# Performance work log

Hardware: AMD Instinct MI355X
Metric: run time of the kernel (lower is better)

The kernel has to match this reference:

```python
import jax, jax.numpy as jnp
import numpy as np
import math

B, N = 1, 768
C_S, C_Z, C_H, H, P_QK, P_V = 256, 128, 128, 8, 8, 12
EPS, INF, LN_EPS = 1e-8, 1e5, 1e-5


def _quat_to_rot(q):
    # q: [..., 4] normalized quaternion (w, x, y, z) -> [..., 3, 3]
    w, x, y, z = jnp.moveaxis(q, -1, 0)
    r = jnp.stack([
        1 - 2 * (y * y + z * z), 2 * (x * y - w * z), 2 * (x * z + w * y),
        2 * (x * y + w * z), 1 - 2 * (x * x + z * z), 2 * (y * z - w * x),
        2 * (x * z - w * y), 2 * (y * z + w * x), 1 - 2 * (x * x + y * y),
    ], axis=-1)
    return r.reshape(q.shape[:-1] + (3, 3))


def _ln(x, g, b):
    mu = x.mean(-1, keepdims=True)
    var = ((x - mu) ** 2).mean(-1, keepdims=True)
    return (x - mu) * jax.lax.rsqrt(var + LN_EPS) * g + b


def setup_inputs():
    key = jax.random.key(0)
    ks = jax.random.split(key, 20)
    inp = {}
    inp['s'] = jax.random.normal(ks[0], (B, N, C_S), jnp.float32)
    inp['p'] = jax.random.normal(ks[1], (B, N, N, C_Z), jnp.float32)
    q = jax.random.normal(ks[2], (B, N, 4), jnp.float32)
    inp['rot'] = _quat_to_rot(q / jnp.linalg.norm(q, axis=-1, keepdims=True))
    inp['trans'] = 10.0 * jax.random.normal(ks[3], (B, N, 3), jnp.float32)
    inp['mask'] = jnp.ones((B, N), jnp.float32)
    concat_dim = H * C_H + H * P_V * 4 + H * C_Z
    dims = {'q': (H * C_H, C_S), 'kv': (2 * H * C_H, C_S), 'qp': (H * P_QK * 3, C_S),
            'kvp': (H * (P_QK + P_V) * 3, C_S), 'pb': (H, C_Z), 'o': (C_S, concat_dim),
            't1': (C_S, C_S), 't2': (C_S, C_S), 't3': (C_S, C_S), 'bb': (6, C_S)}
    i = 4
    for nm, (do, di) in dims.items():
        k1, k2 = jax.random.split(ks[i]); i += 1
        inp['W' + nm] = 0.02 * jax.random.normal(k1, (do, di), jnp.float32)
        inp['b' + nm] = 0.02 * jax.random.normal(k2, (do,), jnp.float32)
    inp['head_w'] = 0.1 * jax.random.normal(ks[i], (H,), jnp.float32)
    inp['g1'] = jnp.ones((C_S,), jnp.float32)
    inp['be1'] = jnp.zeros((C_S,), jnp.float32)
    inp['g2'] = jnp.ones((C_S,), jnp.float32)
    inp['be2'] = jnp.zeros((C_S,), jnp.float32)
    return inp


def reference(s, p, rot, trans, mask, Wq, bq, Wkv, bkv, Wqp, bqp, Wkvp, bkvp,
              Wpb, bpb, Wo, bo, Wt1, bt1, Wt2, bt2, Wt3, bt3, Wbb, bbb,
              head_w, g1, be1, g2, be2):
    # ---------------- Invariant Point Attention ----------------
    q = (s @ Wq.T + bq).reshape(B, N, H, C_H)
    kv = (s @ Wkv.T + bkv).reshape(B, N, H, 2 * C_H)
    k, v = kv[..., :C_H], kv[..., C_H:]
    # points: linear output is coordinate-major (x-block, y-block, z-block)
    qp = (s @ Wqp.T + bqp).reshape(B, N, 3, H, P_QK)
    qp = jnp.einsum('bnij,bnjhp->bnhpi', rot, qp) + trans[:, :, None, None, :]
    kvp = (s @ Wkvp.T + bkvp).reshape(B, N, 3, H, P_QK + P_V)
    kvp = jnp.einsum('bnij,bnjhp->bnhpi', rot, kvp) + trans[:, :, None, None, :]
    kp, vp = kvp[..., :P_QK, :], kvp[..., P_QK:, :]
    bias_p = p @ Wpb.T + bpb  # [B,N,N,H]
    a = jnp.einsum('bihc,bjhc->bhij', q, k) * math.sqrt(1.0 / (3 * C_H))
    a = a + math.sqrt(1.0 / 3) * jnp.transpose(bias_p, (0, 3, 1, 2))
    d2 = ((qp[:, :, None] - kp[:, None]) ** 2).sum(-1)  # [B,N,N,H,Pqk]
    hw = jax.nn.softplus(head_w) * math.sqrt(1.0 / (3 * (P_QK * 9.0 / 2)))
    pt_att = -0.5 * (d2 * hw[None, None, None, :, None]).sum(-1)  # [B,N,N,H]
    m2 = mask[:, :, None] * mask[:, None, :]
    a = a + jnp.transpose(pt_att, (0, 3, 1, 2)) + (INF * (m2 - 1.0))[:, None]
    att = jax.nn.softmax(a, axis=-1)  # [B,H,N,N]
    o = jnp.einsum('bhij,bjhc->bihc', att, v).reshape(B, N, H * C_H)
    opt = jnp.einsum('bhij,bjhpx->bihpx', att, vp)  # [B,N,H,Pv,3] global
    opt = jnp.einsum('bnji,bnhpj->bnhpi', rot, opt - trans[:, :, None, None, :])
    opt_norm = jnp.sqrt((opt ** 2).sum(-1) + EPS).reshape(B, N, H * P_V)
    opt_flat = jnp.moveaxis(opt.reshape(B, N, H * P_V, 3), -1, -2).reshape(B, N, 3 * H * P_V)
    opair = jnp.einsum('bhij,bijz->bihz', att, p).reshape(B, N, H * C_Z)
    ipa_out = jnp.concatenate([o, opt_flat, opt_norm, opair], -1) @ Wo.T + bo
    # residual + dropout(eval: identity) + LayerNorm
    s1 = _ln(s + ipa_out, g1, be1)
    # ---------------- StructureTransition (1 layer) ----------------
    x = jax.nn.relu(s1 @ Wt1.T + bt1)
    x = jax.nn.relu(x @ Wt2.T + bt2)
    s2 = _ln(s1 + (x @ Wt3.T + bt3), g2, be2)
    # ---------------- BackboneUpdate + masked quaternion compose ----------------
    upd = (s2 @ Wbb.T + bbb) * mask[..., None]  # [B,N,6]
    qvec = jnp.concatenate([jnp.ones(upd.shape[:-1] + (1,), upd.dtype), upd[..., :3]], -1)
    qvec = qvec / jnp.linalg.norm(qvec, axis=-1, keepdims=True)
    rot_new = jnp.einsum('bnij,bnjk->bnik', rot, _quat_to_rot(qvec))
    trans_new = trans + jnp.einsum('bnij,bnj->bni', rot, upd[..., 3:])
    return (s2, rot_new, trans_new)
```

## Files before the change

### kernel.cpp

```cpp
#include <hip/hip_runtime.h>
#include <hip/hip_bf16.h>
#include <math.h>

#define NN 768
#define CS 256
#define CZ 128
#define CH 128
#define HH 8
#define PQK 8
#define PV 12
#define CONCAT 2432
#define ATT_HSTRIDE (768*768)

typedef __bf16 v8bf __attribute__((ext_vector_type(8)));
typedef float  v4f  __attribute__((ext_vector_type(4)));

__device__ inline unsigned short f2bf(float f) {
    union { float f; unsigned u; } v; v.f = f;
    unsigned r = v.u + 0x7FFFu + ((v.u >> 16) & 1u);
    return (unsigned short)(r >> 16);
}
__device__ inline float bf2f(unsigned short u) {
    union { unsigned u; float f; } v; v.u = ((unsigned)u) << 16; return v.f;
}

#define NCVT 9
struct CvtDesc {
    const float* src[NCVT];
    unsigned short* dst[NCVT];
    int nelem[NCVT];
    int blk_start[NCVT + 1];
};

__global__ __launch_bounds__(256) void cvt_many(CvtDesc d)
{
    int b = blockIdx.x;
    int seg = 0;
    #pragma unroll
    for (int i = 0; i < NCVT - 1; i++) if (b >= d.blk_start[i + 1]) seg = i + 1;
    int local = b - d.blk_start[seg];
    int base = local * 2048 + threadIdx.x;
    const float* s = d.src[seg];
    unsigned short* o = d.dst[seg];
    int n = d.nelem[seg];
    #pragma unroll
    for (int r = 0; r < 8; r++) {
        int idx = base + r * 256;
        if (idx < n) o[idx] = f2bf(s[idx]);
    }
}

template<int SPLITK, int MODE, int RELU>
__global__ __launch_bounds__(256) void mfma_gemm(
    const unsigned short* __restrict__ A,
    const unsigned short* __restrict__ W,
    const float* __restrict__ bias,
    float* __restrict__ C,
    unsigned short* __restrict__ Cb,
    int D, int K, int ldc)
{
    __shared__ unsigned short As[64][40];
    __shared__ unsigned short Ws[64][40];
    int tid = threadIdx.x;
    int bi = blockIdx.y * 64;
    int bd = blockIdx.x * 64;
    int kpb = K / SPLITK;
    int k0b = blockIdx.z * kpb;
    int lane = tid & 63;
    int wid = tid >> 6;
    int wr = (wid >> 1) * 32, wc = (wid & 1) * 32;
    v4f acc[2][2] = {};
    int lrow = tid >> 2;
    int lcol = (tid & 3) * 8;
    const unsigned short* Ap = A + (size_t)(bi + lrow) * K + lcol;
    const unsigned short* Wp = W + (size_t)(bd + lrow) * K + lcol;
    bool wv = (bd + lrow) < D;
    int fr = lane & 15, fc = (lane >> 4) * 8;

    for (int k0 = k0b; k0 < k0b + kpb; k0 += 32) {
        *(int4*)&As[lrow][lcol] = *(const int4*)(Ap + k0);
        int4 wz = {0, 0, 0, 0};
        *(int4*)&Ws[lrow][lcol] = wv ? *(const int4*)(Wp + k0) : wz;
        __syncthreads();
        v8bf a0 = *(const v8bf*)&As[wr + fr][fc];
        v8bf a1 = *(const v8bf*)&As[wr + 16 + fr][fc];
        v8bf b0 = *(const v8bf*)&Ws[wc + fr][fc];
        v8bf b1 = *(const v8bf*)&Ws[wc + 16 + fr][fc];
        acc[0][0] = __builtin_amdgcn_mfma_f32_16x16x32_bf16(a0, b0, acc[0][0], 0, 0, 0);
        acc[0][1] = __builtin_amdgcn_mfma_f32_16x16x32_bf16(a0, b1, acc[0][1], 0, 0, 0);
        acc[1][0] = __builtin_amdgcn_mfma_f32_16x16x32_bf16(a1, b0, acc[1][0], 0, 0, 0);
        acc[1][1] = __builtin_amdgcn_mfma_f32_16x16x32_bf16(a1, b1, acc[1][1], 0, 0, 0);
        __syncthreads();
    }
    int mrow = (lane >> 4) * 4;
    #pragma unroll
    for (int mi = 0; mi < 2; mi++) {
        #pragma unroll
        for (int ni = 0; ni < 2; ni++) {
            int d = bd + wc + ni * 16 + fr;
            if (d < D) {
                #pragma unroll
                for (int r = 0; r < 4; r++) {
                    int m = bi + wr + mi * 16 + mrow + r;
                    float v = acc[mi][ni][r];
                    if (SPLITK > 1) {
                        atomicAdd(&C[(size_t)m * ldc + d], v);
                    } else {
                        v += bias[d];
                        if (RELU) v = fmaxf(v, 0.f);
                        if (MODE != 2) C[(size_t)m * ldc + d] = v;
                        if (MODE >= 1) Cb[(size_t)m * ldc + d] = f2bf(v);
                    }
                }
            }
        }
    }
}

__global__ __launch_bounds__(256) void ipa_init_kernel(
    const float* __restrict__ bo, float* __restrict__ ipa)
{
    ipa[blockIdx.x * 256 + threadIdx.x] = bo[threadIdx.x];
}

__global__ void prep_kernel(const float* __restrict__ head_w, float* __restrict__ hw8)
{
    int t = threadIdx.x;
    if (t < HH) {
        float x = head_w[t];
        float sp = (x > 20.f) ? x : log1pf(expf(x));
        hw8[t] = sp * 0.09622504486493764f;
    }
}

__global__ void rotate_kernel(
    const float* __restrict__ qpraw, const float* __restrict__ kvpraw,
    const float* __restrict__ rot, const float* __restrict__ trans,
    float* __restrict__ qpb, float* __restrict__ kpb,
    unsigned short* __restrict__ qph, unsigned short* __restrict__ qpl,
    unsigned short* __restrict__ kph, unsigned short* __restrict__ kpl,
    unsigned short* __restrict__ Vc)
{
    int id = blockIdx.x*256 + threadIdx.x;
    if (id >= NN*HH*28) return;
    int i = id / (HH*28);
    int rem = id % (HH*28);
    int h = rem / 28;
    int idx = rem % 28;
    const float* R = rot + i*9;
    const float* T = trans + i*3;
    float s0, s1, s2;
    if (idx < 8) {
        s0 = qpraw[i*192 +   0 + h*8 + idx];
        s1 = qpraw[i*192 +  64 + h*8 + idx];
        s2 = qpraw[i*192 + 128 + h*8 + idx];
    } else {
        int pp = idx - 8;
        s0 = kvpraw[i*480 +   0 + h*20 + pp];
        s1 = kvpraw[i*480 + 160 + h*20 + pp];
        s2 = kvpraw[i*480 + 320 + h*20 + pp];
    }
    float ov[3];
    ov[0] = R[0]*s0 + R[1]*s1 + R[2]*s2 + T[0];
    ov[1] = R[3]*s0 + R[4]*s1 + R[5]*s2 + T[1];
    ov[2] = R[6]*s0 + R[7]*s1 + R[8]*s2 + T[2];
    if (idx < 8) {
        #pragma unroll
        for (int x = 0; x < 3; x++) {
            qpb[i*192 + h*24 + idx*3 + x] = ov[x];
            unsigned short hi = f2bf(ov[x]);
            qph[i*256 + h*32 + idx*3 + x] = hi;
            qpl[i*256 + h*32 + idx*3 + x] = f2bf(ov[x] - bf2f(hi));
        }
        if (idx == 0) {
            #pragma unroll
            for (int m = 24; m < 32; m++) { qph[i*256+h*32+m] = 0; qpl[i*256+h*32+m] = 0; }
        }
    } else if (idx < 16) {
        int pp = idx - 8;
        #pragma unroll
        for (int x = 0; x < 3; x++) {
            kpb[i*192 + h*24 + pp*3 + x] = ov[x];
            unsigned short hi = f2bf(ov[x]);
            kph[i*256 + h*32 + pp*3 + x] = hi;
            kpl[i*256 + h*32 + pp*3 + x] = f2bf(ov[x] - bf2f(hi));
        }
        if (idx == 8) {
            #pragma unroll
            for (int m = 24; m < 32; m++) { kph[i*256+h*32+m] = 0; kpl[i*256+h*32+m] = 0; }
        }
    } else {
        int ppv = idx - 16;
        #pragma unroll
        for (int x = 0; x < 3; x++)
            Vc[((size_t)h*192 + 128 + ppv*3 + x)*768 + i] = f2bf(ov[x]);
    }
}

__global__ void sq_kernel(const float* __restrict__ qpb, const float* __restrict__ kpb,
                          float* __restrict__ Qsq, float* __restrict__ Ksq)
{
    int id = blockIdx.x*256 + threadIdx.x;
    if (id >= NN*HH) return;
    const float* qq = qpb + id*24;
    const float* kk = kpb + id*24;
    float a = 0.f, b = 0.f;
    #pragma unroll
    for (int m = 0; m < 24; m++) { a += qq[m]*qq[m]; b += kk[m]*kk[m]; }
    Qsq[id] = a; Ksq[id] = b;
}

__global__ __launch_bounds__(256) void vtrans_kernel(
    const unsigned short* __restrict__ kv_bf, unsigned short* __restrict__ Vc)
{
    __shared__ unsigned short tile[32][136];
    int h = blockIdx.x & 7, jt = blockIdx.x >> 3;
    int t = threadIdx.x;
    int r = t >> 3, c0 = (t & 7) * 16;
    const unsigned short* src = kv_bf + (size_t)(jt*32 + r)*2048 + h*256 + 128 + c0;
    *(int4*)&tile[r][c0]     = *(const int4*)src;
    *(int4*)&tile[r][c0 + 8] = *(const int4*)(src + 8);
    __syncthreads();
    int c = t >> 1, jh = (t & 1) * 16;
    unsigned short tmp[16];
    #pragma unroll
    for (int k = 0; k < 16; k++) tmp[k] = tile[jh + k][c];
    unsigned short* dst = Vc + ((size_t)h*192 + c)*768 + jt*32 + jh;
    *(int4*)dst       = *(int4*)&tmp[0];
    *(int4*)(dst + 8) = *(int4*)&tmp[8];
}

__global__ __launch_bounds__(256) void logits_mfma(
    const unsigned short* __restrict__ q_bf, const unsigned short* __restrict__ kv_bf,
    const unsigned short* __restrict__ qph, const unsigned short* __restrict__ qpl,
    const unsigned short* __restrict__ kph, const unsigned short* __restrict__ kpl,
    const float* __restrict__ Qsq, const float* __restrict__ Ksq,
    const float* __restrict__ mask, const float* __restrict__ hw8,
    float* __restrict__ att)
{
    __shared__ unsigned short Qs[64][136];
    __shared__ unsigned short Ks[64][136];
    __shared__ unsigned short Aph[64][40], Apl[64][40], Bph[64][40], Bpl[64][40];
    __shared__ float Qss[64], Kss[64], Mi[64], Mj[64];
    int h = blockIdx.z;
    int i0 = blockIdx.y * 64, j0 = blockIdx.x * 64;
    int tid = threadIdx.x, lane = tid & 63, wid = tid >> 6;
    int wr = (wid >> 1) * 32, wc = (wid & 1) * 32;
    int r = tid >> 2, cq = (tid & 3) * 32;
    const unsigned short* qg = q_bf  + (size_t)(i0 + r)*1024 + h*128 + cq;
    const unsigned short* kg = kv_bf + (size_t)(j0 + r)*2048 + h*256 + cq;
    #pragma unroll
    for (int kk = 0; kk < 4; kk++) {
        *(int4*)&Qs[r][cq + kk*8] = *(const int4*)(qg + kk*8);
        *(int4*)&Ks[r][cq + kk*8] = *(const int4*)(kg + kk*8);
    }
    int cp = (tid & 3) * 8;
    *(int4*)&Aph[r][cp] = *(const int4*)(qph + (size_t)(i0 + r)*256 + h*32 + cp);
    *(int4*)&Apl[r][cp] = *(const int4*)(qpl + (size_t)(i0 + r)*256 + h*32 + cp);
    *(int4*)&Bph[r][cp] = *(const int4*)(kph + (size_t)(j0 + r)*256 + h*32 + cp);
    *(int4*)&Bpl[r][cp] = *(const int4*)(kpl + (size_t)(j0 + r)*256 + h*32 + cp);
    if (tid < 64) {
        Qss[tid] = Qsq[(i0 + tid)*8 + h];
        Kss[tid] = Ksq[(j0 + tid)*8 + h];
        Mi[tid] = mask[i0 + tid];
        Mj[tid] = mask[j0 + tid];
    }
    __syncthreads();
    int fr = lane & 15, fc = (lane >> 4) * 8;
    v4f aqk[2][2] = {}, ap[2][2] = {};
    #pragma unroll
    for (int ks = 0; ks < 4; ks++) {
        v8bf a0 = *(const v8bf*)&Qs[wr + fr][ks*32 + fc];
        v8bf a1 = *(const v8bf*)&Qs[wr + 16 + fr][ks*32 + fc];
        v8bf b0 = *(const v8bf*)&Ks[wc + fr][ks*32 + fc];
        v8bf b1 = *(const v8bf*)&Ks[wc + 16 + fr][ks*32 + fc];
        aqk[0][0] = __builtin_amdgcn_mfma_f32_16x16x32_bf16(a0, b0, aqk[0][0], 0, 0, 0);
        aqk[0][1] = __builtin_amdgcn_mfma_f32_16x16x32_bf16(a0, b1, aqk[0][1], 0, 0, 0);
        aqk[1][0] = __builtin_amdgcn_mfma_f32_16x16x32_bf16(a1, b0, aqk[1][0], 0, 0, 0);
        aqk[1][1] = __builtin_amdgcn_mfma_f32_16x16x32_bf16(a1, b1, aqk[1][1], 0, 0, 0);
    }
    {
        v8bf ah0 = *(const v8bf*)&Aph[wr + fr][fc];
        v8bf ah1 = *(const v8bf*)&Aph[wr + 16 + fr][fc];
        v8bf al0 = *(const v8bf*)&Apl[wr + fr][fc];
        v8bf al1 = *(const v8bf*)&Apl[wr + 16 + fr][fc];
        v8bf bh0 = *(const v8bf*)&Bph[wc + fr][fc];
        v8bf bh1 = *(const v8bf*)&Bph[wc + 16 + fr][fc];
        v8bf bl0 = *(const v8bf*)&Bpl[wc + fr][fc];
        v8bf bl1 = *(const v8bf*)&Bpl[wc + 16 + fr][fc];
        ap[0][0] = __builtin_amdgcn_mfma_f32_16x16x32_bf16(ah0, bh0, ap[0][0], 0, 0, 0);
        ap[0][1] = __builtin_amdgcn_mfma_f32_16x16x32_bf16(ah0, bh1, ap[0][1], 0, 0, 0);
        ap[1][0] = __builtin_amdgcn_mfma_f32_16x16x32_bf16(ah1, bh0, ap[1][0], 0, 0, 0);
        ap[1][1] = __builtin_amdgcn_mfma_f32_16x16x32_bf16(ah1, bh1, ap[1][1], 0, 0, 0);
        ap[0][0] = __builtin_amdgcn_mfma_f32_16x16x32_bf16(ah0, bl0, ap[0][0], 0, 0, 0);
        ap[0][1] = __builtin_amdgcn_mfma_f32_16x16x32_bf16(ah0, bl1, ap[0][1], 0, 0, 0);
        ap[1][0] = __builtin_amdgcn_mfma_f32_16x16x32_bf16(ah1, bl0, ap[1][0], 0, 0, 0);
        ap[1][1] = __builtin_amdgcn_mfma_f32_16x16x32_bf16(ah1, bl1, ap[1][1], 0, 0, 0);
        ap[0][0] = __builtin_amdgcn_mfma_f32_16x16x32_bf16(al0, bh0, ap[0][0], 0, 0, 0);
        ap[0][1] = __builtin_amdgcn_mfma_f32_16x16x32_bf16(al0, bh1, ap[0][1], 0, 0, 0);
        ap[1][0] = __builtin_amdgcn_mfma_f32_16x16x32_bf16(al1, bh0, ap[1][0], 0, 0, 0);
        ap[1][1] = __builtin_amdgcn_mfma_f32_16x16x32_bf16(al1, bh1, ap[1][1], 0, 0, 0);
    }
    float hw = hw8[h];
    const float scale_qk = 0.05103103630798288f;
    int mrow = (lane >> 4) * 4;
    #pragma unroll
    for (int mi = 0; mi < 2; mi++) {
        #pragma unroll
        for (int ni = 0; ni < 2; ni++) {
            int jl = wc + ni*16 + fr;
            #pragma unroll
            for (int rr = 0; rr < 4; rr++) {
                int il = wr + mi*16 + mrow + rr;
                size_t aidx = (size_t)h*ATT_HSTRIDE + (size_t)(i0 + il)*768 + (j0 + jl);
                att[aidx] = aqk[mi][ni][rr]*scale_qk + hw*ap[mi][ni][rr]
                          - 0.5f*hw*(Qss[il] + Kss[jl])
                          + 100000.0f*(Mi[il]*Mj[jl] - 1.0f);
            }
        }
    }
}

__global__ __launch_bounds__(256) void fused_p2_kernel(
    const float* __restrict__ att0,
    const float* __restrict__ p,
    const float* __restrict__ Wpb, const float* __restrict__ bpb,
    unsigned short* __restrict__ att_bf,
    float* __restrict__ linv,
    unsigned short* __restrict__ concat)
{
    __shared__ unsigned short ptile[64][136];
    __shared__ unsigned short pT[128][88];
    __shared__ unsigned short wt[16][72];
    __shared__ unsigned short Wpb16[16][136];
    __shared__ float bpb_s[8], m8[8], inv_s[8], lsum_w[4][8];

    int i = blockIdx.x;
    int tid = threadIdx.x, lane = tid & 63, wid = tid >> 6;
    int fr = lane & 15, fc = (lane >> 4) * 8;
    int mrow = (lane >> 4) * 4;

    for (int idx = tid; idx < 16*72; idx += 256) wt[idx / 72][idx % 72] = 0;
    for (int idx = tid; idx < 16*136; idx += 256) {
        int h = idx / 136, z = idx % 136;
        Wpb16[h][z] = (h < 8 && z < 128) ? f2bf(Wpb[h*128 + z]) : 0;
    }
    if (tid < 8) bpb_s[tid] = bpb[tid];

    {
        const float* abase = att0 + (size_t)i*768;
        #pragma unroll
        for (int hh = 0; hh < 2; hh++) {
            int h = wid*2 + hh;
            const float* row = abase + (size_t)h*ATT_HSTRIDE;
            float m = -3.0e38f;
            #pragma unroll
            for (int e = 0; e < 12; e++) m = fmaxf(m, row[lane + e*64]);
            #pragma unroll
            for (int d2 = 1; d2 < 64; d2 <<= 1) m = fmaxf(m, __shfl_xor(m, d2));
            if (lane == 0) m8[h] = m;
        }
    }

    const float* pbase = p + (size_t)i*98304;
    float4 pfA[4], pfB[4];
    #pragma unroll
    for (int r = 0; r < 4; r++) {
        int idx = r*256 + tid;
        const float* src = pbase + (idx >> 4)*128 + (idx & 15)*8;
        pfA[r] = *(const float4*)src;
        pfB[r] = *(const float4*)(src + 4);
    }

    v4f accop[2] = {};
    float lacc[4] = {0.f, 0.f, 0.f, 0.f};
    const float sqrt13 = 0.57735026918962576f;

    for (int t64 = 0; t64 < 12; t64++) {
        int j0 = t64 * 64;
        #pragma unroll
        for (int r = 0; r < 4; r++) {
            int idx = r*256 + tid;
            int j = idx >> 4, zo = (idx & 15) * 8;
            unsigned u0 = (unsigned)f2bf(pfA[r].x) | ((unsigned)f2bf(pfA[r].y) << 16);
            unsigned u1 = (unsigned)f2bf(pfA[r].z) | ((unsigned)f2bf(pfA[r].w) << 16);
            unsigned u2 = (unsigned)f2bf(pfB[r].x) | ((unsigned)f2bf(pfB[r].y) << 16);
            unsigned u3 = (unsigned)f2bf(pfB[r].z) | ((unsigned)f2bf(pfB[r].w) << 16);
            int4 val; val.x = (int)u0; val.y = (int)u1; val.z = (int)u2; val.w = (int)u3;
            *(int4*)&ptile[j][zo] = val;
        }
        if (t64 < 11) {
            int j0n = j0 + 64;
            #pragma unroll
            for (int r = 0; r < 4; r++) {
                int idx = r*256 + tid;
                const float* src = pbase + (size_t)(j0n + (idx >> 4))*128 + (idx & 15)*8;
                pfA[r] = *(const float4*)src;
                pfB[r] = *(const float4*)(src + 4);
            }
        }
        __syncthreads();

        float a0v[4];
        if (mrow < 8) {
            int j = 16*wid + fr;
            #pragma unroll
            for (int r = 0; r < 4; r++)
                a0v[r] = att0[((size_t)(mrow + r)*768 + i)*768 + j0 + j];
        }

        #pragma unroll
        for (int rep = 0; rep < 2; rep++) {
            int item = rep*256 + tid;
            int zp = item & 63, jg = item >> 6;
            unsigned v[8];
            #pragma unroll
            for (int k = 0; k < 8; k++)
                v[k] = *(const unsigned*)&ptile[jg*8 + k][zp*2];
            unsigned r0[4], r1[4];
            #pragma unroll
            for (int q = 0; q < 4; q++) {
                unsigned a = v[2*q], b = v[2*q + 1];
                r0[q] = (a & 0xffffu) | ((b & 0xffffu) << 16);
                r1[q] = (a >> 16) | (b & 0xffff0000u);
            }
            int4 w0; w0.x = (int)r0[0]; w0.y = (int)r0[1]; w0.z = (int)r0[2]; w0.w = (int)r0[3];
            int4 w1; w1.x = (int)r1[0]; w1.y = (int)r1[1]; w1.z = (int)r1[2]; w1.w = (int)r1[3];
            *(int4*)&pT[2*zp][jg*8]     = w0;
            *(int4*)&pT[2*zp + 1][jg*8] = w1;
        }

        v4f bd = {};
        #pragma unroll
        for (int ks = 0; ks < 4; ks++) {
            v8bf a = *(const v8bf*)&Wpb16[fr][ks*32 + fc];
            v8bf b = *(const v8bf*)&ptile[16*wid + fr][ks*32 + fc];
            bd = __builtin_amdgcn_mfma_f32_16x16x32_bf16(a, b, bd, 0, 0, 0);
        }

        if (mrow < 8) {
            int j = 16*wid + fr;
            float w8[4];
            #pragma unroll
            for (int r = 0; r < 4; r++) {
                int h = mrow + r;
                float L = a0v[r] + sqrt13*(bd[r] + bpb_s[h]);
                w8[r] = expf(fminf(L - m8[h], 60.f));
            }
            #pragma unroll
            for (int r = 0; r < 4; r++) {
                int h = mrow + r;
                unsigned short wb = f2bf(w8[r]);
                wt[h][j] = wb;
                att_bf[((size_t)h*768 + i)*768 + j0 + j] = wb;
            }
            #pragma unroll
            for (int m = 1; m < 16; m <<= 1) {
                #pragma unroll
                for (int r = 0; r < 4; r++) w8[r] += __shfl_xor(w8[r], m);
            }
            #pragma unroll
            for (int r = 0; r < 4; r++) lacc[r] += w8[r];
        }
        __syncthreads();

        #pragma unroll
        for (int mm = 0; mm < 2; mm++) {
            #pragma unroll
            for (int ks = 0; ks < 2; ks++) {
                v8bf a = *(const v8bf*)&pT[(2*wid + mm)*16 + fr][ks*32 + fc];
                v8bf b = *(const v8bf*)&wt[fr][ks*32 + fc];
                accop[mm] = __builtin_amdgcn_mfma_f32_16x16x32_bf16(a, b, accop[mm], 0, 0, 0);
            }
        }
    }

    __syncthreads();
    if (fr == 0 && mrow < 8) {
        #pragma unroll
        for (int r = 0; r < 4; r++) lsum_w[wid][mrow + r] = lacc[r];
    }
    __syncthreads();
    if (tid < 8) {
        float l = lsum_w[0][tid] + lsum_w[1][tid] + lsum_w[2][tid] + lsum_w[3][tid];
        float iv = 1.0f / l;
        inv_s[tid] = iv;
        linv[(size_t)tid*768 + i] = iv;
    }
    __syncthreads();
    if (fr < 8) {
        int h = fr;
        float iv = inv_s[h];
        #pragma unroll
        for (int mm = 0; mm < 2; mm++) {
            #pragma unroll
            for (int r = 0; r < 4; r++) {
                int z = (2*wid + mm)*16 + mrow + r;
                concat[(size_t)i*CONCAT + 1408 + h*128 + z] = f2bf(accop[mm][r] * iv);
            }
        }
    }
}

__global__ __launch_bounds__(256) void attvc_mfma(
    const unsigned short* __restrict__ att_bf, const unsigned short* __restrict__ Vc,
    const float* __restrict__ linv,
    unsigned short* __restrict__ concat, float* __restrict__ optb)
{
    __shared__ unsigned short As[64][72];
    __shared__ unsigned short Bs[64][72];
    int h = blockIdx.z;
    int i0 = blockIdx.y * 64, nd0 = blockIdx.x * 64;
    int tid = threadIdx.x, lane = tid & 63, wid = tid >> 6;
    int wr = (wid >> 1) * 32, wc = (wid & 1) * 32;
    int r = tid >> 2, c8 = (tid & 3) * 16;
    int fr = lane & 15, fc = (lane >> 4) * 8;
    v4f acc[2][2] = {};
    for (int k0 = 0; k0 < 768; k0 += 64) {
        const unsigned short* ag = att_bf + ((size_t)h*768 + i0 + r)*768 + k0 + c8;
        const unsigned short* bg = Vc + ((size_t)h*192 + nd0 + r)*768 + k0 + c8;
        *(int4*)&As[r][c8]     = *(const int4*)ag;
        *(int4*)&As[r][c8 + 8] = *(const int4*)(ag + 8);
        *(int4*)&Bs[r][c8]     = *(const int4*)bg;
        *(int4*)&Bs[r][c8 + 8] = *(const int4*)(bg + 8);
        __syncthreads();
        #pragma unroll
        for (int ks = 0; ks < 2; ks++) {
            v8bf a0 = *(const v8bf*)&As[wr + fr][ks*32 + fc];
            v8bf a1 = *(const v8bf*)&As[wr + 16 + fr][ks*32 + fc];
            v8bf b0 = *(const v8bf*)&Bs[wc + fr][ks*32 + fc];
            v8bf b1 = *(const v8bf*)&Bs[wc + 16 + fr][ks*32 + fc];
            acc[0][0] = __builtin_amdgcn_mfma_f32_16x16x32_bf16(a0, b0, acc[0][0], 0, 0, 0);
            acc[0][1] = __builtin_amdgcn_mfma_f32_16x16x32_bf16(a0, b1, acc[0][1], 0, 0, 0);
            acc[1][0] = __builtin_amdgcn_mfma_f32_16x16x32_bf16(a1, b0, acc[1][0], 0, 0, 0);
            acc[1][1] = __builtin_amdgcn_mfma_f32_16x16x32_bf16(a1, b1, acc[1][1], 0, 0, 0);
        }
        __syncthreads();
    }
    int mrow = (lane >> 4) * 4;
    float lv[2][4];
    #pragma unroll
    for (int mi = 0; mi < 2; mi++) {
        int ibase = i0 + wr + mi*16 + mrow;
        float4 l4 = *(const float4*)&linv[(size_t)h*768 + ibase];
        lv[mi][0] = l4.x; lv[mi][1] = l4.y; lv[mi][2] = l4.z; lv[mi][3] = l4.w;
    }
    #pragma unroll
    for (int mi = 0; mi < 2; mi++) {
        #pragma unroll
        for (int ni = 0; ni < 2; ni++) {
            int d = nd0 + wc + ni*16 + fr;
            #pragma unroll
            for (int rr = 0; rr < 4; rr++) {
                int i = i0 + wr + mi*16 + mrow + rr;
                float v = acc[mi][ni][rr] * lv[mi][rr];
                if (d < 128) {
                    concat[(size_t)i*CONCAT + h*128 + d] = f2bf(v);
                } else if (d < 164) {
                    optb[(size_t)i*288 + h*36 + (d - 128)] = v;
                }
            }
        }
    }
}

__global__ void optfinal_kernel(
    const float* __restrict__ optb, const float* __restrict__ rot,
    const float* __restrict__ trans, unsigned short* __restrict__ concat)
{
    int id = blockIdx.x*256 + threadIdx.x;
    if (id >= NN*96) return;
    int i = id / 96;
    int hp = id % 96;
    const float* ob = optb + i*288 + hp*3;
    float y0 = ob[0] - trans[i*3+0];
    float y1 = ob[1] - trans[i*3+1];
    float y2 = ob[2] - trans[i*3+2];
    const float* R = rot + i*9;
    float o0 = R[0]*y0 + R[3]*y1 + R[6]*y2;
    float o1 = R[1]*y0 + R[4]*y1 + R[7]*y2;
    float o2 = R[2]*y0 + R[5]*y1 + R[8]*y2;
    float nrm = sqrtf(o0*o0 + o1*o1 + o2*o2 + 1e-8f);
    unsigned short* cb = concat + (size_t)i*CONCAT;
    cb[1024 +   0 + hp] = f2bf(o0);
    cb[1024 +  96 + hp] = f2bf(o1);
    cb[1024 + 192 + hp] = f2bf(o2);
    cb[1312 + hp] = f2bf(nrm);
}

template<int BF>
__global__ __launch_bounds__(256) void add_ln_kernel(
    const float* __restrict__ A, const float* __restrict__ Bv,
    const float* __restrict__ g, const float* __restrict__ be,
    float* __restrict__ out, unsigned short* __restrict__ outb)
{
    int i = blockIdx.x, t = threadIdx.x;
    float x = A[i*256 + t] + Bv[i*256 + t];
    __shared__ float red[4];
    float v = x;
    #pragma unroll
    for (int m = 1; m < 64; m <<= 1) v += __shfl_xor(v, m);
    if ((t & 63) == 0) red[t >> 6] = v;
    __syncthreads();
    float mu = (red[0] + red[1] + red[2] + red[3]) * (1.0f/256.0f);
    __syncthreads();
    float d = x - mu;
    float v2 = d*d;
    #pragma unroll
    for (int m = 1; m < 64; m <<= 1) v2 += __shfl_xor(v2, m);
    if ((t & 63) == 0) red[t >> 6] = v2;
    __syncthreads();
    float var = (red[0] + red[1] + red[2] + red[3]) * (1.0f/256.0f);
    float o = d * (1.0f/sqrtf(var + 1e-5f)) * g[t] + be[t];
    out[i*256 + t] = o;
    if (BF) outb[i*256 + t] = f2bf(o);
}

__global__ __launch_bounds__(256) void upd_kernel(
    const float* __restrict__ s2, const float* __restrict__ Wbb,
    const float* __restrict__ bbb, const float* __restrict__ mask,
    float* __restrict__ upd)
{
    int i = blockIdx.x, t = threadIdx.x;
    __shared__ float row[256];
    row[t] = s2[i*256 + t];
    __syncthreads();
    if (t < 6) {
        float acc = bbb[t];
        #pragma unroll 8
        for (int c = 0; c < 256; c++) acc += row[c]*Wbb[t*256 + c];
        upd[i*6 + t] = acc * mask[i];
    }
}

__global__ void frame_kernel(
    const float* __restrict__ upd, const float* __restrict__ rot,
    const float* __restrict__ trans, float* __restrict__ rot_out,
    float* __restrict__ trans_out)
{
    int i = blockIdx.x*64 + threadIdx.x;
    if (i >= NN) return;
    float u0 = upd[i*6+0], u1 = upd[i*6+1], u2 = upd[i*6+2];
    float t0 = upd[i*6+3], t1 = upd[i*6+4], t2 = upd[i*6+5];
    float n = sqrtf(1.f + u0*u0 + u1*u1 + u2*u2);
    float w = 1.f/n, x = u0/n, y = u1/n, z = u2/n;
    float R[3][3];
    R[0][0] = 1.f - 2.f*(y*y + z*z); R[0][1] = 2.f*(x*y - w*z);       R[0][2] = 2.f*(x*z + w*y);
    R[1][0] = 2.f*(x*y + w*z);       R[1][1] = 1.f - 2.f*(x*x + z*z); R[1][2] = 2.f*(y*z - w*x);
    R[2][0] = 2.f*(x*z - w*y);       R[2][1] = 2.f*(y*z + w*x);       R[2][2] = 1.f - 2.f*(x*x + y*y);
    const float* Ri = rot + i*9;
    #pragma unroll
    for (int a = 0; a < 3; a++) {
        #pragma unroll
        for (int b = 0; b < 3; b++) {
            float acc = 0.f;
            #pragma unroll
            for (int j = 0; j < 3; j++) acc += Ri[a*3+j]*R[j][b];
            rot_out[i*9 + a*3 + b] = acc;
        }
        trans_out[i*3 + a] = trans[i*3 + a] + Ri[a*3+0]*t0 + Ri[a*3+1]*t1 + Ri[a*3+2]*t2;
    }
}

extern "C" void kernel_launch(void* const* d_in, const int* in_sizes, int n_in,
                              void* d_out, int out_size, void* d_ws, size_t ws_size,
                              hipStream_t stream)
{
    const float* s      = (const float*)d_in[0];
    const float* p      = (const float*)d_in[1];
    const float* rot    = (const float*)d_in[2];
    const float* trans  = (const float*)d_in[3];
    const float* mask   = (const float*)d_in[4];
    const float* Wq     = (const float*)d_in[5];
    const float* bq     = (const float*)d_in[6];
    const float* Wkv    = (const float*)d_in[7];
    const float* bkv    = (const float*)d_in[8];
    const float* Wqp    = (const float*)d_in[9];
    const float* bqp    = (const float*)d_in[10];
    const float* Wkvp   = (const float*)d_in[11];
    const float* bkvp   = (const float*)d_in[12];
    const float* Wpb    = (const float*)d_in[13];
    const float* bpb    = (const float*)d_in[14];
    const float* Wo     = (const float*)d_in[15];
    const float* bo     = (const float*)d_in[16];
    const float* Wt1    = (const float*)d_in[17];
    const float* bt1    = (const float*)d_in[18];
    const float* Wt2    = (const float*)d_in[19];
    const float* bt2    = (const float*)d_in[20];
    const float* Wt3    = (const float*)d_in[21];
    const float* bt3    = (const float*)d_in[22];
    const float* Wbb    = (const float*)d_in[23];
    const float* bbb    = (const float*)d_in[24];
    const float* head_w = (const float*)d_in[25];
    const float* g1     = (const float*)d_in[26];
    const float* be1    = (const float*)d_in[27];
    const float* g2     = (const float*)d_in[28];
    const float* be2    = (const float*)d_in[29];

    float* out = (float*)d_out;
    char*  wsb = (char*)d_ws;

    size_t off = 0;
    auto alloc = [&](size_t bytes) -> char* {
        char* ptr = wsb + off;
        off += (bytes + 255) & ~(size_t)255;
        return ptr;
    };
    float* qpraw   = (float*)alloc((size_t)NN*192*4);
    float* kvpraw  = (float*)alloc((size_t)NN*480*4);
    float* qpb     = (float*)alloc((size_t)NN*192*4);
    float* kpb     = (float*)alloc((size_t)NN*192*4);
    float* Qsq     = (float*)alloc((size_t)NN*8*4);
    float* Ksq     = (float*)alloc((size_t)NN*8*4);
    float* hw8     = (float*)alloc(64);
    float* att     = (float*)alloc((size_t)8*768*768*4);
    float* optb    = (float*)alloc((size_t)NN*288*4);
    float* ipa     = (float*)alloc((size_t)NN*256*4);
    float* s1      = (float*)alloc((size_t)NN*256*4);
    float* y3      = (float*)alloc((size_t)NN*256*4);
    float* updb    = (float*)alloc((size_t)NN*6*4);
    float* linv    = (float*)alloc((size_t)8*768*4);
    unsigned short* s_bf    = (unsigned short*)alloc((size_t)NN*256*2);
    unsigned short* Wq_bf   = (unsigned short*)alloc((size_t)1024*256*2);
    unsigned short* Wkv_bf  = (unsigned short*)alloc((size_t)2048*256*2);
    unsigned short* Wqp_bf  = (unsigned short*)alloc((size_t)192*256*2);
    unsigned short* Wkvp_bf = (unsigned short*)alloc((size_t)480*256*2);
    unsigned short* Wo_bf   = (unsigned short*)alloc((size_t)256*2432*2);
    unsigned short* Wt1_bf  = (unsigned short*)alloc((size_t)256*256*2);
    unsigned short* Wt2_bf  = (unsigned short*)alloc((size_t)256*256*2);
    unsigned short* Wt3_bf  = (unsigned short*)alloc((size_t)256*256*2);
    unsigned short* q_bf    = (unsigned short*)alloc((size_t)NN*1024*2);
    unsigned short* kv_bf   = (unsigned short*)alloc((size_t)NN*2048*2);
    unsigned short* qph     = (unsigned short*)alloc((size_t)NN*256*2);
    unsigned short* qpl     = (unsigned short*)alloc((size_t)NN*256*2);
    unsigned short* kph     = (unsigned short*)alloc((size_t)NN*256*2);
    unsigned short* kpl     = (unsigned short*)alloc((size_t)NN*256*2);
    unsigned short* Vc      = (unsigned short*)alloc((size_t)8*192*768*2);
    unsigned short* att_bf  = (unsigned short*)alloc((size_t)8*768*768*2);
    unsigned short* concat  = (unsigned short*)alloc((size_t)NN*CONCAT*2);
    unsigned short* s1b     = (unsigned short*)alloc((size_t)NN*256*2);
    unsigned short* x1b     = (unsigned short*)alloc((size_t)NN*256*2);
    unsigned short* x2b     = (unsigned short*)alloc((size_t)NN*256*2);

    CvtDesc cd;
    const float* csrc[NCVT]    = {s, Wq, Wkv, Wqp, Wkvp, Wo, Wt1, Wt2, Wt3};
    unsigned short* cdst[NCVT] = {s_bf, Wq_bf, Wkv_bf, Wqp_bf, Wkvp_bf, Wo_bf, Wt1_bf, Wt2_bf, Wt3_bf};
    int csz[NCVT] = {NN*256, 1024*256, 2048*256, 192*256, 480*256, 256*2432, 256*256, 256*256, 256*256};
    int cum = 0;
    for (int i2 = 0; i2 < NCVT; i2++) {
        cd.src[i2] = csrc[i2]; cd.dst[i2] = cdst[i2]; cd.nelem[i2] = csz[i2];
        cd.blk_start[i2] = cum;
        cum += (csz[i2] + 2047) / 2048;
    }
    cd.blk_start[NCVT] = cum;
    cvt_many<<<cum, 256, 0, stream>>>(cd);

    mfma_gemm<1,2,0><<<dim3(16,12), 256, 0, stream>>>(s_bf, Wq_bf,   bq,   nullptr, q_bf,  1024, 256, 1024);
    mfma_gemm<1,2,0><<<dim3(32,12), 256, 0, stream>>>(s_bf, Wkv_bf,  bkv,  nullptr, kv_bf, 2048, 256, 2048);
    mfma_gemm<1,0,0><<<dim3(3,12),  256, 0, stream>>>(s_bf, Wqp_bf,  bqp,  qpraw,  nullptr, 192, 256, 192);
    mfma_gemm<1,0,0><<<dim3(8,12),  256, 0, stream>>>(s_bf, Wkvp_bf, bkvp, kvpraw, nullptr, 480, 256, 480);

    prep_kernel<<<1, 64, 0, stream>>>(head_w, hw8);
    rotate_kernel<<<(NN*HH*28 + 255)/256, 256, 0, stream>>>(
        qpraw, kvpraw, rot, trans, qpb, kpb, qph, qpl, kph, kpl, Vc);
    sq_kernel<<<(NN*HH + 255)/256, 256, 0, stream>>>(qpb, kpb, Qsq, Ksq);
    vtrans_kernel<<<8*24, 256, 0, stream>>>(kv_bf, Vc);

    logits_mfma<<<dim3(12, 12, 8), 256, 0, stream>>>(
        q_bf, kv_bf, qph, qpl, kph, kpl, Qsq, Ksq, mask, hw8, att);
    fused_p2_kernel<<<768, 256, 0, stream>>>(att, p, Wpb, bpb, att_bf, linv, concat);

    attvc_mfma<<<dim3(3, 12, 8), 256, 0, stream>>>(att_bf, Vc, linv, concat, optb);
    optfinal_kernel<<<(NN*96 + 255)/256, 256, 0, stream>>>(optb, rot, trans, concat);

    ipa_init_kernel<<<768, 256, 0, stream>>>(bo, ipa);
    mfma_gemm<4,0,0><<<dim3(4,12,4), 256, 0, stream>>>(concat, Wo_bf, nullptr, ipa, nullptr, 256, 2432, 256);
    add_ln_kernel<1><<<768, 256, 0, stream>>>(s, ipa, g1, be1, s1, s1b);

    mfma_gemm<1,2,1><<<dim3(4,12), 256, 0, stream>>>(s1b, Wt1_bf, bt1, nullptr, x1b, 256, 256, 256);
    mfma_gemm<1,2,1><<<dim3(4,12), 256, 0, stream>>>(x1b, Wt2_bf, bt2, nullptr, x2b, 256, 256, 256);
    mfma_gemm<1,0,0><<<dim3(4,12), 256, 0, stream>>>(x2b, Wt3_bf, bt3, y3, nullptr, 256, 256, 256);
    add_ln_kernel<0><<<768, 256, 0, stream>>>(s1, y3, g2, be2, out, nullptr);

    upd_kernel<<<768, 256, 0, stream>>>(out, Wbb, bbb, mask, updb);
    frame_kernel<<<12, 64, 0, stream>>>(updb, rot, trans, out + (size_t)NN*256, out + (size_t)NN*256 + (size_t)NN*9);
}
```

Baseline: 213.7 us.

## Fuse projections, squared-norm, softplus, opt-final and frame kernels; drop pT transpose

Merges the four input projection GEMMs into one grouped launch and folds the squared-norm, head-weight softplus, output-point rotation and frame update into neighbouring kernels. This removes several small launches and their intermediate buffers. The pair-bias kernel no longer builds a transposed copy in shared memory; it reads columns directly for the MFMA B operand and keeps Wpb in registers. It also switches to the fast exp and native bf16 conversions. Squared norms are now rebuilt from the hi/lo bf16 split, which may slightly change precision, and the strided shared-memory column reads may cause bank conflicts.

```diff
diff --git a/kernel.cpp b/kernel.cpp
--- a/kernel.cpp
+++ b/kernel.cpp
@@ -13,6 +13,7 @@
 #define ATT_HSTRIDE (768*768)
 
 typedef __bf16 v8bf __attribute__((ext_vector_type(8)));
+typedef __bf16 v4bf __attribute__((ext_vector_type(4)));
 typedef float  v4f  __attribute__((ext_vector_type(4)));
 
 __device__ inline unsigned short f2bf(float f) {
@@ -47,6 +48,77 @@
     for (int r = 0; r < 8; r++) {
         int idx = base + r * 256;
         if (idx < n) o[idx] = f2bf(s[idx]);
+    }
+}
+
+struct ProjDesc {
+    const unsigned short* W[4];
+    const float* bias[4];
+    unsigned short* dstb[4];
+    float* dstf[4];
+    int D[4];
+    int ldc[4];
+    int mode[4];
+    int blk_start[5];
+};
+
+__global__ __launch_bounds__(256) void proj_all(const unsigned short* __restrict__ A, ProjDesc d)
+{
+    __shared__ unsigned short As[64][40];
+    __shared__ unsigned short Ws[64][40];
+    int bx = blockIdx.x;
+    int seg = 0;
+    #pragma unroll
+    for (int q = 0; q < 3; q++) if (bx >= d.blk_start[q + 1]) seg = q + 1;
+    int bd = (bx - d.blk_start[seg]) * 64;
+    int bi = blockIdx.y * 64;
+    const unsigned short* W = d.W[seg];
+    int D = d.D[seg], ldc = d.ldc[seg];
+
+    int tid = threadIdx.x, lane = tid & 63, wid = tid >> 6;
+    int wr = (wid >> 1) * 32, wc = (wid & 1) * 32;
+    v4f acc[2][2] = {};
+    int lrow = tid >> 2, lcol = (tid & 3) * 8;
+    const unsigned short* Ap = A + (size_t)(bi + lrow) * 256 + lcol;
+    const unsigned short* Wp = W + (size_t)(bd + lrow) * 256 + lcol;
+    bool wv = (bd + lrow) < D;
+    int fr = lane & 15, fc = (lane >> 4) * 8;
+
+    for (int k0 = 0; k0 < 256; k0 += 32) {
+        *(int4*)&As[lrow][lcol] = *(const int4*)(Ap + k0);
+        int4 wz = {0, 0, 0, 0};
+        *(int4*)&Ws[lrow][lcol] = wv ? *(const int4*)(Wp + k0) : wz;
+        __syncthreads();
+        v8bf a0 = *(const v8bf*)&As[wr + fr][fc];
+        v8bf a1 = *(const v8bf*)&As[wr + 16 + fr][fc];
+        v8bf b0 = *(const v8bf*)&Ws[wc + fr][fc];
+        v8bf b1 = *(const v8bf*)&Ws[wc + 16 + fr][fc];
+        acc[0][0] = __builtin_amdgcn_mfma_f32_16x16x32_bf16(a0, b0, acc[0][0], 0, 0, 0);
+        acc[0][1] = __builtin_amdgcn_mfma_f32_16x16x32_bf16(a0, b1, acc[0][1], 0, 0, 0);
+        acc[1][0] = __builtin_amdgcn_mfma_f32_16x16x32_bf16(a1, b0, acc[1][0], 0, 0, 0);
+        acc[1][1] = __builtin_amdgcn_mfma_f32_16x16x32_bf16(a1, b1, acc[1][1], 0, 0, 0);
+        __syncthreads();
+    }
+    const float* bias = d.bias[seg];
+    int mode = d.mode[seg];
+    unsigned short* Cb = d.dstb[seg];
+    float* Cf = d.dstf[seg];
+    int mrow = (lane >> 4) * 4;
+    #pragma unroll
+    for (int mi = 0; mi < 2; mi++) {
+        #pragma unroll
+        for (int ni = 0; ni < 2; ni++) {
+            int dd = bd + wc + ni * 16 + fr;
+            if (dd < D) {
+                #pragma unroll
+                for (int r = 0; r < 4; r++) {
+                    int m = bi + wr + mi * 16 + mrow + r;
+                    float v = acc[mi][ni][r] + bias[dd];
+                    if (mode == 2) Cb[(size_t)m * ldc + dd] = f2bf(v);
+                    else           Cf[(size_t)m * ldc + dd] = v;
+                }
+            }
+        }
     }
 }
 
@@ -123,20 +195,9 @@
     ipa[blockIdx.x * 256 + threadIdx.x] = bo[threadIdx.x];
 }
 
-__global__ void prep_kernel(const float* __restrict__ head_w, float* __restrict__ hw8)
-{
-    int t = threadIdx.x;
-    if (t < HH) {
-        float x = head_w[t];
-        float sp = (x > 20.f) ? x : log1pf(expf(x));
-        hw8[t] = sp * 0.09622504486493764f;
-    }
-}
-
 __global__ void rotate_kernel(
     const float* __restrict__ qpraw, const float* __restrict__ kvpraw,
     const float* __restrict__ rot, const float* __restrict__ trans,
-    float* __restrict__ qpb, float* __restrict__ kpb,
     unsigned short* __restrict__ qph, unsigned short* __restrict__ qpl,
     unsigned short* __restrict__ kph, unsigned short* __restrict__ kpl,
     unsigned short* __restrict__ Vc)
@@ -167,7 +228,6 @@
     if (idx < 8) {
         #pragma unroll
         for (int x = 0; x < 3; x++) {
-            qpb[i*192 + h*24 + idx*3 + x] = ov[x];
             unsigned short hi = f2bf(ov[x]);
             qph[i*256 + h*32 + idx*3 + x] = hi;
             qpl[i*256 + h*32 + idx*3 + x] = f2bf(ov[x] - bf2f(hi));
@@ -180,7 +240,6 @@
         int pp = idx - 8;
         #pragma unroll
         for (int x = 0; x < 3; x++) {
-            kpb[i*192 + h*24 + pp*3 + x] = ov[x];
             unsigned short hi = f2bf(ov[x]);
             kph[i*256 + h*32 + pp*3 + x] = hi;
             kpl[i*256 + h*32 + pp*3 + x] = f2bf(ov[x] - bf2f(hi));
@@ -195,19 +254,6 @@
         for (int x = 0; x < 3; x++)
             Vc[((size_t)h*192 + 128 + ppv*3 + x)*768 + i] = f2bf(ov[x]);
     }
-}
-
-__global__ void sq_kernel(const float* __restrict__ qpb, const float* __restrict__ kpb,
-                          float* __restrict__ Qsq, float* __restrict__ Ksq)
-{
-    int id = blockIdx.x*256 + threadIdx.x;
-    if (id >= NN*HH) return;
-    const float* qq = qpb + id*24;
-    const float* kk = kpb + id*24;
-    float a = 0.f, b = 0.f;
-    #pragma unroll
-    for (int m = 0; m < 24; m++) { a += qq[m]*qq[m]; b += kk[m]*kk[m]; }
-    Qsq[id] = a; Ksq[id] = b;
 }
 
 __global__ __launch_bounds__(256) void vtrans_kernel(
@@ -234,8 +280,7 @@
     const unsigned short* __restrict__ q_bf, const unsigned short* __restrict__ kv_bf,
     const unsigned short* __restrict__ qph, const unsigned short* __restrict__ qpl,
     const unsigned short* __restrict__ kph, const unsigned short* __restrict__ kpl,
-    const float* __restrict__ Qsq, const float* __restrict__ Ksq,
-    const float* __restrict__ mask, const float* __restrict__ hw8,
+    const float* __restrict__ mask, const float* __restrict__ head_w,
     float* __restrict__ att)
 {
     __shared__ unsigned short Qs[64][136];
@@ -260,12 +305,20 @@
     *(int4*)&Bph[r][cp] = *(const int4*)(kph + (size_t)(j0 + r)*256 + h*32 + cp);
     *(int4*)&Bpl[r][cp] = *(const int4*)(kpl + (size_t)(j0 + r)*256 + h*32 + cp);
     if (tid < 64) {
-        Qss[tid] = Qsq[(i0 + tid)*8 + h];
-        Kss[tid] = Ksq[(j0 + tid)*8 + h];
         Mi[tid] = mask[i0 + tid];
         Mj[tid] = mask[j0 + tid];
     }
     __syncthreads();
+    if (tid < 64) {
+        float qs2 = 0.f, ks2 = 0.f;
+        #pragma unroll
+        for (int m = 0; m < 24; m++) {
+            float qv = bf2f(Aph[tid][m]) + bf2f(Apl[tid][m]);
+            float kv = bf2f(Bph[tid][m]) + bf2f(Bpl[tid][m]);
+            qs2 += qv*qv; ks2 += kv*kv;
+        }
+        Qss[tid] = qs2; Kss[tid] = ks2;
+    }
     int fr = lane & 15, fc = (lane >> 4) * 8;
     v4f aqk[2][2] = {}, ap[2][2] = {};
     #pragma unroll
@@ -301,7 +354,10 @@
         ap[1][0] = __builtin_amdgcn_mfma_f32_16x16x32_bf16(al1, bh0, ap[1][0], 0, 0, 0);
         ap[1][1] = __builtin_amdgcn_mfma_f32_16x16x32_bf16(al1, bh1, ap[1][1], 0, 0, 0);
     }
-    float hw = hw8[h];
+    __syncthreads();
+    float hx = head_w[h];
+    float sp = (hx > 20.f) ? hx : log1pf(__expf(hx));
+    float hw = sp * 0.09622504486493764f;
     const float scale_qk = 0.05103103630798288f;
     int mrow = (lane >> 4) * 4;
     #pragma unroll
@@ -321,7 +377,7 @@
     }
 }
 
-__global__ __launch_bounds__(256) void fused_p2_kernel(
+__global__ __launch_bounds__(256) void fused_p3_kernel(
     const float* __restrict__ att0,
     const float* __restrict__ p,
     const float* __restrict__ Wpb, const float* __restrict__ bpb,
@@ -329,10 +385,8 @@
     float* __restrict__ linv,
     unsigned short* __restrict__ concat)
 {
-    __shared__ unsigned short ptile[64][136];
-    __shared__ unsigned short pT[128][88];
+    __shared__ unsigned short ptile[64][132];
     __shared__ unsigned short wt[16][72];
-    __shared__ unsigned short Wpb16[16][136];
     __shared__ float bpb_s[8], m8[8], inv_s[8], lsum_w[4][8];
 
     int i = blockIdx.x;
@@ -340,12 +394,22 @@
     int fr = lane & 15, fc = (lane >> 4) * 8;
     int mrow = (lane >> 4) * 4;
 
-    for (int idx = tid; idx < 16*72; idx += 256) wt[idx / 72][idx % 72] = 0;
-    for (int idx = tid; idx < 16*136; idx += 256) {
-        int h = idx / 136, z = idx % 136;
-        Wpb16[h][z] = (h < 8 && z < 128) ? f2bf(Wpb[h*128 + z]) : 0;
-    }
+    for (int idx = tid; idx < 16*72; idx += 256) ((unsigned short*)wt)[idx] = 0;
     if (tid < 8) bpb_s[tid] = bpb[tid];
+
+    v8bf aW[4];
+    #pragma unroll
+    for (int ks = 0; ks < 4; ks++) {
+        v8bf v = {};
+        if (fr < 8) {
+            const float* wp = Wpb + fr*128 + ks*32 + fc;
+            float4 w0 = *(const float4*)wp;
+            float4 w1 = *(const float4*)(wp + 4);
+            v[0] = (__bf16)w0.x; v[1] = (__bf16)w0.y; v[2] = (__bf16)w0.z; v[3] = (__bf16)w0.w;
+            v[4] = (__bf16)w1.x; v[5] = (__bf16)w1.y; v[6] = (__bf16)w1.z; v[7] = (__bf16)w1.w;
+        }
+        aW[ks] = v;
+    }
 
     {
         const float* abase = att0 + (size_t)i*768;
@@ -361,6 +425,13 @@
             if (lane == 0) m8[h] = m;
         }
     }
+    __syncthreads();
+    float m0a[4], m0b[4];
+    #pragma unroll
+    for (int r = 0; r < 4; r++) { m0a[r] = m8[r]; m0b[r] = m8[4 + r]; }
+    float m0l[4];
+    #pragma unroll
+    for (int r = 0; r < 4; r++) m0l[r] = (mrow == 0) ? m0a[r] : m0b[r];
 
     const float* pbase = p + (size_t)i*98304;
     float4 pfA[4], pfB[4];
@@ -372,9 +443,10 @@
         pfB[r] = *(const float4*)(src + 4);
     }
 
-    v4f accop[2] = {};
+    v4f accD[2] = {};
     float lacc[4] = {0.f, 0.f, 0.f, 0.f};
     const float sqrt13 = 0.57735026918962576f;
+    bool expo = (mrow < 8);
 
     for (int t64 = 0; t64 < 12; t64++) {
         int j0 = t64 * 64;
@@ -382,12 +454,13 @@
         for (int r = 0; r < 4; r++) {
             int idx = r*256 + tid;
             int j = idx >> 4, zo = (idx & 15) * 8;
-            unsigned u0 = (unsigned)f2bf(pfA[r].x) | ((unsigned)f2bf(pfA[r].y) << 16);
-            unsigned u1 = (unsigned)f2bf(pfA[r].z) | ((unsigned)f2bf(pfA[r].w) << 16);
-            unsigned u2 = (unsigned)f2bf(pfB[r].x) | ((unsigned)f2bf(pfB[r].y) << 16);
-            unsigned u3 = (unsigned)f2bf(pfB[r].z) | ((unsigned)f2bf(pfB[r].w) << 16);
-            int4 val; val.x = (int)u0; val.y = (int)u1; val.z = (int)u2; val.w = (int)u3;
-            *(int4*)&ptile[j][zo] = val;
+            v4bf lo, hi;
+            lo[0] = (__bf16)pfA[r].x; lo[1] = (__bf16)pfA[r].y;
+            lo[2] = (__bf16)pfA[r].z; lo[3] = (__bf16)pfA[r].w;
+            hi[0] = (__bf16)pfB[r].x; hi[1] = (__bf16)pfB[r].y;
+            hi[2] = (__bf16)pfB[r].z; hi[3] = (__bf16)pfB[r].w;
+            *(v4bf*)&ptile[j][zo]     = lo;
+            *(v4bf*)&ptile[j][zo + 4] = hi;
         }
         if (t64 < 11) {
             int j0n = j0 + 64;
@@ -402,50 +475,33 @@
         __syncthreads();
 
         float a0v[4];
-        if (mrow < 8) {
+        if (expo) {
             int j = 16*wid + fr;
             #pragma unroll
             for (int r = 0; r < 4; r++)
                 a0v[r] = att0[((size_t)(mrow + r)*768 + i)*768 + j0 + j];
         }
 
-        #pragma unroll
-        for (int rep = 0; rep < 2; rep++) {
-            int item = rep*256 + tid;
-            int zp = item & 63, jg = item >> 6;
-            unsigned v[8];
-            #pragma unroll
-            for (int k = 0; k < 8; k++)
-                v[k] = *(const unsigned*)&ptile[jg*8 + k][zp*2];
-            unsigned r0[4], r1[4];
-            #pragma unroll
-            for (int q = 0; q < 4; q++) {
-                unsigned a = v[2*q], b = v[2*q + 1];
-                r0[q] = (a & 0xffffu) | ((b & 0xffffu) << 16);
-                r1[q] = (a >> 16) | (b & 0xffff0000u);
-            }
-            int4 w0; w0.x = (int)r0[0]; w0.y = (int)r0[1]; w0.z = (int)r0[2]; w0.w = (int)r0[3];
-            int4 w1; w1.x = (int)r1[0]; w1.y = (int)r1[1]; w1.z = (int)r1[2]; w1.w = (int)r1[3];
-            *(int4*)&pT[2*zp][jg*8]     = w0;
-            *(int4*)&pT[2*zp + 1][jg*8] = w1;
-        }
-
         v4f bd = {};
         #pragma unroll
         for (int ks = 0; ks < 4; ks++) {
-            v8bf a = *(const v8bf*)&Wpb16[fr][ks*32 + fc];
-            v8bf b = *(const v8bf*)&ptile[16*wid + fr][ks*32 + fc];
-            bd = __builtin_amdgcn_mfma_f32_16x16x32_bf16(a, b, bd, 0, 0, 0);
-        }
-
-        if (mrow < 8) {
+            int c = ks*32 + fc;
+            v4bf blo = *(const v4bf*)&ptile[16*wid + fr][c];
+            v4bf bhi = *(const v4bf*)&ptile[16*wid + fr][c + 4];
+            v8bf b;
+            b[0]=blo[0]; b[1]=blo[1]; b[2]=blo[2]; b[3]=blo[3];
+            b[4]=bhi[0]; b[5]=bhi[1]; b[6]=bhi[2]; b[7]=bhi[3];
+            bd = __builtin_amdgcn_mfma_f32_16x16x32_bf16(aW[ks], b, bd, 0, 0, 0);
+        }
+
+        if (expo) {
             int j = 16*wid + fr;
             float w8[4];
             #pragma unroll
             for (int r = 0; r < 4; r++) {
                 int h = mrow + r;
                 float L = a0v[r] + sqrt13*(bd[r] + bpb_s[h]);
-                w8[r] = expf(fminf(L - m8[h], 60.f));
+                w8[r] = __expf(fminf(L - m0l[r], 60.f));
             }
             #pragma unroll
             for (int r = 0; r < 4; r++) {
@@ -466,17 +522,21 @@
 
         #pragma unroll
         for (int mm = 0; mm < 2; mm++) {
+            int zcol = (2*wid + mm)*16 + fr;
             #pragma unroll
             for (int ks = 0; ks < 2; ks++) {
-                v8bf a = *(const v8bf*)&pT[(2*wid + mm)*16 + fr][ks*32 + fc];
-                v8bf b = *(const v8bf*)&wt[fr][ks*32 + fc];
-                accop[mm] = __builtin_amdgcn_mfma_f32_16x16x32_bf16(a, b, accop[mm], 0, 0, 0);
-            }
-        }
-    }
-
-    __syncthreads();
-    if (fr == 0 && mrow < 8) {
+                v8bf b;
+                #pragma unroll
+                for (int kk = 0; kk < 8; kk++)
+                    b[kk] = *(const __bf16*)&ptile[ks*32 + fc + kk][zcol];
+                v8bf a = *(const v8bf*)&wt[fr][ks*32 + fc];
+                accD[mm] = __builtin_amdgcn_mfma_f32_16x16x32_bf16(a, b, accD[mm], 0, 0, 0);
+            }
+        }
+        __syncthreads();
+    }
+
+    if (fr == 0 && expo) {
         #pragma unroll
         for (int r = 0; r < 4; r++) lsum_w[wid][mrow + r] = lacc[r];
     }
@@ -488,15 +548,14 @@
         linv[(size_t)tid*768 + i] = iv;
     }
     __syncthreads();
-    if (fr < 8) {
-        int h = fr;
-        float iv = inv_s[h];
+    if (expo) {
         #pragma unroll
         for (int mm = 0; mm < 2; mm++) {
+            int z = (2*wid + mm)*16 + fr;
             #pragma unroll
             for (int r = 0; r < 4; r++) {
-                int z = (2*wid + mm)*16 + mrow + r;
-                concat[(size_t)i*CONCAT + 1408 + h*128 + z] = f2bf(accop[mm][r] * iv);
+                int h = mrow + r;
+                concat[(size_t)i*CONCAT + 1408 + h*128 + z] = f2bf(accD[mm][r] * inv_s[h]);
             }
         }
     }
@@ -504,8 +563,8 @@
 
 __global__ __launch_bounds__(256) void attvc_mfma(
     const unsigned short* __restrict__ att_bf, const unsigned short* __restrict__ Vc,
-    const float* __restrict__ linv,
-    unsigned short* __restrict__ concat, float* __restrict__ optb)
+    const float* __restrict__ linv, const float* __restrict__ rot,
+    const float* __restrict__ trans, unsigned short* __restrict__ concat)
 {
     __shared__ unsigned short As[64][72];
     __shared__ unsigned short Bs[64][72];
@@ -545,47 +604,56 @@
         float4 l4 = *(const float4*)&linv[(size_t)h*768 + ibase];
         lv[mi][0] = l4.x; lv[mi][1] = l4.y; lv[mi][2] = l4.z; lv[mi][3] = l4.w;
     }
-    #pragma unroll
-    for (int mi = 0; mi < 2; mi++) {
-        #pragma unroll
-        for (int ni = 0; ni < 2; ni++) {
-            int d = nd0 + wc + ni*16 + fr;
-            #pragma unroll
-            for (int rr = 0; rr < 4; rr++) {
-                int i = i0 + wr + mi*16 + mrow + rr;
-                float v = acc[mi][ni][rr] * lv[mi][rr];
-                if (d < 128) {
-                    concat[(size_t)i*CONCAT + h*128 + d] = f2bf(v);
-                } else if (d < 164) {
-                    optb[(size_t)i*288 + h*36 + (d - 128)] = v;
+    if (nd0 < 128) {
+        #pragma unroll
+        for (int mi = 0; mi < 2; mi++) {
+            #pragma unroll
+            for (int ni = 0; ni < 2; ni++) {
+                int d = nd0 + wc + ni*16 + fr;
+                #pragma unroll
+                for (int rr = 0; rr < 4; rr++) {
+                    int i = i0 + wr + mi*16 + mrow + rr;
+                    concat[(size_t)i*CONCAT + h*128 + d] = f2bf(acc[mi][ni][rr] * lv[mi][rr]);
                 }
             }
         }
-    }
-}
-
-__global__ void optfinal_kernel(
-    const float* __restrict__ optb, const float* __restrict__ rot,
-    const float* __restrict__ trans, unsigned short* __restrict__ concat)
-{
-    int id = blockIdx.x*256 + threadIdx.x;
-    if (id >= NN*96) return;
-    int i = id / 96;
-    int hp = id % 96;
-    const float* ob = optb + i*288 + hp*3;
-    float y0 = ob[0] - trans[i*3+0];
-    float y1 = ob[1] - trans[i*3+1];
-    float y2 = ob[2] - trans[i*3+2];
-    const float* R = rot + i*9;
-    float o0 = R[0]*y0 + R[3]*y1 + R[6]*y2;
-    float o1 = R[1]*y0 + R[4]*y1 + R[7]*y2;
-    float o2 = R[2]*y0 + R[5]*y1 + R[8]*y2;
-    float nrm = sqrtf(o0*o0 + o1*o1 + o2*o2 + 1e-8f);
-    unsigned short* cb = concat + (size_t)i*CONCAT;
-    cb[1024 +   0 + hp] = f2bf(o0);
-    cb[1024 +  96 + hp] = f2bf(o1);
-    cb[1024 + 192 + hp] = f2bf(o2);
-    cb[1312 + hp] = f2bf(nrm);
+    } else {
+        float* opt_s = (float*)&As[0][0];
+        #pragma unroll
+        for (int mi = 0; mi < 2; mi++) {
+            #pragma unroll
+            for (int ni = 0; ni < 2; ni++) {
+                int c = wc + ni*16 + fr;
+                if (c < 36) {
+                    #pragma unroll
+                    for (int rr = 0; rr < 4; rr++) {
+                        int rl = wr + mi*16 + mrow + rr;
+                        opt_s[rl*36 + c] = acc[mi][ni][rr] * lv[mi][rr];
+                    }
+                }
+            }
+        }
+        __syncthreads();
+        for (int it = tid; it < 768; it += 256) {
+            int rl = it / 12, pp = it % 12;
+            int i = i0 + rl;
+            const float* R = rot + i*9;
+            const float* T = trans + i*3;
+            float y0 = opt_s[rl*36 + pp*3 + 0] - T[0];
+            float y1 = opt_s[rl*36 + pp*3 + 1] - T[1];
+            float y2 = opt_s[rl*36 + pp*3 + 2] - T[2];
+            float o0 = R[0]*y0 + R[3]*y1 + R[6]*y2;
+            float o1 = R[1]*y0 + R[4]*y1 + R[7]*y2;
+            float o2 = R[2]*y0 + R[5]*y1 + R[8]*y2;
+            float nrm = sqrtf(o0*o0 + o1*o1 + o2*o2 + 1e-8f);
+            int hp = h*12 + pp;
+            unsigned short* cb = concat + (size_t)i*CONCAT;
+            cb[1024 +   0 + hp] = f2bf(o0);
+            cb[1024 +  96 + hp] = f2bf(o1);
+            cb[1024 + 192 + hp] = f2bf(o2);
+            cb[1312 + hp] = f2bf(nrm);
+        }
+    }
 }
 
 template<int BF>
@@ -616,49 +684,45 @@
     if (BF) outb[i*256 + t] = f2bf(o);
 }
 
-__global__ __launch_bounds__(256) void upd_kernel(
+__global__ __launch_bounds__(256) void upd_frame_kernel(
     const float* __restrict__ s2, const float* __restrict__ Wbb,
     const float* __restrict__ bbb, const float* __restrict__ mask,
-    float* __restrict__ upd)
+    const float* __restrict__ rot, const float* __restrict__ trans,
+    float* __restrict__ rot_out, float* __restrict__ trans_out)
 {
     int i = blockIdx.x, t = threadIdx.x;
     __shared__ float row[256];
+    __shared__ float upd_s[6];
     row[t] = s2[i*256 + t];
     __syncthreads();
     if (t < 6) {
         float acc = bbb[t];
         #pragma unroll 8
         for (int c = 0; c < 256; c++) acc += row[c]*Wbb[t*256 + c];
-        upd[i*6 + t] = acc * mask[i];
-    }
-}
-
-__global__ void frame_kernel(
-    const float* __restrict__ upd, const float* __restrict__ rot,
-    const float* __restrict__ trans, float* __restrict__ rot_out,
-    float* __restrict__ trans_out)
-{
-    int i = blockIdx.x*64 + threadIdx.x;
-    if (i >= NN) return;
-    float u0 = upd[i*6+0], u1 = upd[i*6+1], u2 = upd[i*6+2];
-    float t0 = upd[i*6+3], t1 = upd[i*6+4], t2 = upd[i*6+5];
-    float n = sqrtf(1.f + u0*u0 + u1*u1 + u2*u2);
-    float w = 1.f/n, x = u0/n, y = u1/n, z = u2/n;
-    float R[3][3];
-    R[0][0] = 1.f - 2.f*(y*y + z*z); R[0][1] = 2.f*(x*y - w*z);       R[0][2] = 2.f*(x*z + w*y);
-    R[1][0] = 2.f*(x*y + w*z);       R[1][1] = 1.f - 2.f*(x*x + z*z); R[1][2] = 2.f*(y*z - w*x);
-    R[2][0] = 2.f*(x*z - w*y);       R[2][1] = 2.f*(y*z + w*x);       R[2][2] = 1.f - 2.f*(x*x + y*y);
-    const float* Ri = rot + i*9;
-    #pragma unroll
-    for (int a = 0; a < 3; a++) {
-        #pragma unroll
-        for (int b = 0; b < 3; b++) {
-            float acc = 0.f;
-            #pragma unroll
-            for (int j = 0; j < 3; j++) acc += Ri[a*3+j]*R[j][b];
-            rot_out[i*9 + a*3 + b] = acc;
-        }
-        trans_out[i*3 + a] = trans[i*3 + a] + Ri[a*3+0]*t0 + Ri[a*3+1]*t1 + Ri[a*3+2]*t2;
+        upd_s[t] = acc * mask[i];
+    }
+    __syncthreads();
+    if (t == 0) {
+        float u0 = upd_s[0], u1 = upd_s[1], u2 = upd_s[2];
+        float t0 = upd_s[3], t1 = upd_s[4], t2 = upd_s[5];
+        float n = sqrtf(1.f + u0*u0 + u1*u1 + u2*u2);
+        float w = 1.f/n, x = u0/n, y = u1/n, z = u2/n;
+        float R[3][3];
+        R[0][0] = 1.f - 2.f*(y*y + z*z); R[0][1] = 2.f*(x*y - w*z);       R[0][2] = 2.f*(x*z + w*y);
+        R[1][0] = 2.f*(x*y + w*z);       R[1][1] = 1.f - 2.f*(x*x + z*z); R[1][2] = 2.f*(y*z - w*x);
+        R[2][0] = 2.f*(x*z - w*y);       R[2][1] = 2.f*(y*z + w*x);       R[2][2] = 1.f - 2.f*(x*x + y*y);
+        const float* Ri = rot + i*9;
+        #pragma unroll
+        for (int a = 0; a < 3; a++) {
+            #pragma unroll
+            for (int b = 0; b < 3; b++) {
+                float acc = 0.f;
+                #pragma unroll
+                for (int j = 0; j < 3; j++) acc += Ri[a*3+j]*R[j][b];
+                rot_out[i*9 + a*3 + b] = acc;
+            }
+            trans_out[i*3 + a] = trans[i*3 + a] + Ri[a*3+0]*t0 + Ri[a*3+1]*t1 + Ri[a*3+2]*t2;
+        }
     }
 }
 
@@ -708,17 +772,10 @@
     };
     float* qpraw   = (float*)alloc((size_t)NN*192*4);
     float* kvpraw  = (float*)alloc((size_t)NN*480*4);
-    float* qpb     = (float*)alloc((size_t)NN*192*4);
-    float* kpb     = (float*)alloc((size_t)NN*192*4);
-    float* Qsq     = (float*)alloc((size_t)NN*8*4);
-    float* Ksq     = (float*)alloc((size_t)NN*8*4);
-    float* hw8     = (float*)alloc(64);
     float* att     = (float*)alloc((size_t)8*768*768*4);
-    float* optb    = (float*)alloc((size_t)NN*288*4);
     float* ipa     = (float*)alloc((size_t)NN*256*4);
     float* s1      = (float*)alloc((size_t)NN*256*4);
     float* y3      = (float*)alloc((size_t)NN*256*4);
-    float* updb    = (float*)alloc((size_t)NN*6*4);
     float* linv    = (float*)alloc((size_t)8*768*4);
     unsigned short* s_bf    = (unsigned short*)alloc((size_t)NN*256*2);
     unsigned short* Wq_bf   = (unsigned short*)alloc((size_t)1024*256*2);
@@ -742,6 +799,8 @@
     unsigned short* x1b     = (unsigned short*)alloc((size_t)NN*256*2);
     unsigned short* x2b     = (unsigned short*)alloc((size_t)NN*256*2);
 
+    ipa_init_kernel<<<768, 256, 0, stream>>>(bo, ipa);
+
     CvtDesc cd;
     const float* csrc[NCVT]    = {s, Wq, Wkv, Wqp, Wkvp, Wo, Wt1, Wt2, Wt3};
     unsigned short* cdst[NCVT] = {s_bf, Wq_bf, Wkv_bf, Wqp_bf, Wkvp_bf, Wo_bf, Wt1_bf, Wt2_bf, Wt3_bf};
@@ -755,25 +814,24 @@
     cd.blk_start[NCVT] = cum;
     cvt_many<<<cum, 256, 0, stream>>>(cd);
 
-    mfma_gemm<1,2,0><<<dim3(16,12), 256, 0, stream>>>(s_bf, Wq_bf,   bq,   nullptr, q_bf,  1024, 256, 1024);
-    mfma_gemm<1,2,0><<<dim3(32,12), 256, 0, stream>>>(s_bf, Wkv_bf,  bkv,  nullptr, kv_bf, 2048, 256, 2048);
-    mfma_gemm<1,0,0><<<dim3(3,12),  256, 0, stream>>>(s_bf, Wqp_bf,  bqp,  qpraw,  nullptr, 192, 256, 192);
-    mfma_gemm<1,0,0><<<dim3(8,12),  256, 0, stream>>>(s_bf, Wkvp_bf, bkvp, kvpraw, nullptr, 480, 256, 480);
-
-    prep_kernel<<<1, 64, 0, stream>>>(head_w, hw8);
+    ProjDesc pd;
+    pd.W[0] = Wq_bf;   pd.bias[0] = bq;   pd.dstb[0] = q_bf;   pd.dstf[0] = nullptr; pd.D[0] = 1024; pd.ldc[0] = 1024; pd.mode[0] = 2;
+    pd.W[1] = Wkv_bf;  pd.bias[1] = bkv;  pd.dstb[1] = kv_bf;  pd.dstf[1] = nullptr; pd.D[1] = 2048; pd.ldc[1] = 2048; pd.mode[1] = 2;
+    pd.W[2] = Wqp_bf;  pd.bias[2] = bqp;  pd.dstb[2] = nullptr; pd.dstf[2] = qpraw;  pd.D[2] = 192;  pd.ldc[2] = 192;  pd.mode[2] = 0;
+    pd.W[3] = Wkvp_bf; pd.bias[3] = bkvp; pd.dstb[3] = nullptr; pd.dstf[3] = kvpraw; pd.D[3] = 480;  pd.ldc[3] = 480;  pd.mode[3] = 0;
+    pd.blk_start[0] = 0; pd.blk_start[1] = 16; pd.blk_start[2] = 48; pd.blk_start[3] = 51; pd.blk_start[4] = 59;
+    proj_all<<<dim3(59, 12), 256, 0, stream>>>(s_bf, pd);
+
     rotate_kernel<<<(NN*HH*28 + 255)/256, 256, 0, stream>>>(
-        qpraw, kvpraw, rot, trans, qpb, kpb, qph, qpl, kph, kpl, Vc);
-    sq_kernel<<<(NN*HH + 255)/256, 256, 0, stream>>>(qpb, kpb, Qsq, Ksq);
+        qpraw, kvpraw, rot, trans, qph, qpl, kph, kpl, Vc);
     vtrans_kernel<<<8*24, 256, 0, stream>>>(kv_bf, Vc);
 
     logits_mfma<<<dim3(12, 12, 8), 256, 0, stream>>>(
-        q_bf, kv_bf, qph, qpl, kph, kpl, Qsq, Ksq, mask, hw8, att);
-    fused_p2_kernel<<<768, 256, 0, stream>>>(att, p, Wpb, bpb, att_bf, linv, concat);
-
-    attvc_mfma<<<dim3(3, 12, 8), 256, 0, stream>>>(att_bf, Vc, linv, concat, optb);
-    optfinal_kernel<<<(NN*96 + 255)/256, 256, 0, stream>>>(optb, rot, trans, concat);
-
-    ipa_init_kernel<<<768, 256, 0, stream>>>(bo, ipa);
+        q_bf, kv_bf, qph, qpl, kph, kpl, mask, head_w, att);
+    fused_p3_kernel<<<768, 256, 0, stream>>>(att, p, Wpb, bpb, att_bf, linv, concat);
+
+    attvc_mfma<<<dim3(3, 12, 8), 256, 0, stream>>>(att_bf, Vc, linv, rot, trans, concat);
+
     mfma_gemm<4,0,0><<<dim3(4,12,4), 256, 0, stream>>>(concat, Wo_bf, nullptr, ipa, nullptr, 256, 2432, 256);
     add_ln_kernel<1><<<768, 256, 0, stream>>>(s, ipa, g1, be1, s1, s1b);
 
@@ -782,6 +840,6 @@
     mfma_gemm<1,0,0><<<dim3(4,12), 256, 0, stream>>>(x2b, Wt3_bf, bt3, y3, nullptr, 256, 256, 256);
     add_ln_kernel<0><<<768, 256, 0, stream>>>(s1, y3, g2, be2, out, nullptr);
 
-    upd_kernel<<<768, 256, 0, stream>>>(out, Wbb, bbb, mask, updb);
-    frame_kernel<<<12, 64, 0, stream>>>(updb, rot, trans, out + (size_t)NN*256, out + (size_t)NN*256 + (size_t)NN*9);
-}
+    upd_frame_kernel<<<768, 256, 0, stream>>>(out, Wbb, bbb, mask, rot, trans,
+                                              out + (size_t)NN*256, out + (size_t)NN*256 + (size_t)NN*9);
+}
```

After: 195.1 us. -8.7%, faster.
